# Kernel optimization log

Hardware: AMD Instinct MI355X
Metric: run time of the kernel (lower is better)

The kernel has to match this reference:

```python
import jax, jax.numpy as jnp
import numpy as np
import math

B, T, C = 2, 2048, 1024
H = 16
D = C // H  # 64


def setup_inputs() -> dict:
    key = jax.random.key(0)
    ks = jax.random.split(key, 5)
    s = 0.02
    return {
        "x": jax.random.normal(ks[0], (B, T, C), dtype=jnp.float32),
        "Wqkv": jax.random.normal(ks[1], (C, 3 * C), dtype=jnp.float32) * s,
        "bqkv": jax.random.normal(ks[2], (3 * C,), dtype=jnp.float32) * s,
        "Wo": jax.random.normal(ks[3], (C, C), dtype=jnp.float32) * s,
        "bo": jax.random.normal(ks[4], (C,), dtype=jnp.float32) * s,
    }


def reference(x, Wqkv, bqkv, Wo, bo):
    b, t, c = x.shape
    qkv = x @ Wqkv + bqkv                      # [B,T,3C]
    qkv = qkv.reshape(b, t, 3, H, D)           # split (three h d) as in einops pattern
    q = jnp.transpose(qkv[:, :, 0], (0, 2, 1, 3))  # [B,H,T,D]
    k = jnp.transpose(qkv[:, :, 1], (0, 2, 1, 3))
    v = jnp.transpose(qkv[:, :, 2], (0, 2, 1, 3))
    e = jnp.einsum('bhqd,bhkd->bhqk', q, k) * (1.0 / math.sqrt(D))  # [B,H,T,T]
    causal = jnp.tril(jnp.ones((t, t), dtype=bool))
    e = jnp.where(causal[None, None, :, :], e, -jnp.inf)
    a = jax.nn.softmax(e, axis=-1)             # attention dropout = identity (eval)
    y = jnp.einsum('bhqk,bhkd->bhqd', a, v)    # [B,H,T,D]
    y = jnp.transpose(y, (0, 2, 1, 3)).reshape(b, t, c)
    return y @ Wo + bo                         # resid dropout = identity (eval)
```

## Files before the change

### kernel.cpp

```cpp
#include <hip/hip_runtime.h>
#include <math.h>

#define Bn 2
#define Tn 2048
#define Cn 1024
#define Hn 16
#define Dn 64

typedef short  bf16x8 __attribute__((ext_vector_type(8)));
typedef short  s16x4  __attribute__((ext_vector_type(4)));
typedef float  f32x4  __attribute__((ext_vector_type(4)));

static __device__ __forceinline__ unsigned short f32_bf16(float f) {
    unsigned u = __float_as_uint(f);
    return (unsigned short)((u + 0x7fffu + ((u >> 16) & 1u)) >> 16);
}
static __device__ __forceinline__ float bf16_f32(unsigned short h) {
    return __uint_as_float(((unsigned)h) << 16);
}
static __device__ __forceinline__ void split_store(short* dh, short* dl, float4 v) {
    unsigned short h0 = f32_bf16(v.x), h1 = f32_bf16(v.y),
                   h2 = f32_bf16(v.z), h3 = f32_bf16(v.w);
    *(s16x4*)dh = (s16x4){(short)h0, (short)h1, (short)h2, (short)h3};
    *(s16x4*)dl = (s16x4){(short)f32_bf16(v.x - bf16_f32(h0)),
                          (short)f32_bf16(v.y - bf16_f32(h1)),
                          (short)f32_bf16(v.z - bf16_f32(h2)),
                          (short)f32_bf16(v.w - bf16_f32(h3))};
}

__global__ __launch_bounds__(256) void gemm_mfma3(const float* __restrict__ A,
                                                  const float* __restrict__ B,
                                                  const float* __restrict__ bias,
                                                  float* __restrict__ C,
                                                  int M, int N, int K) {
    __shared__ short Ah[128][40];
    __shared__ short Al[128][40];
    __shared__ short Bh[128][40];
    __shared__ short Bl[128][40];

    const int tid = threadIdx.x;
    const int m0 = blockIdx.y * 128;
    const int n0 = blockIdx.x * 128;
    const int w  = tid >> 6;
    const int l  = tid & 63;
    const int wr = w >> 1;
    const int wc = w & 1;
    const int lr = l & 15;
    const int g8 = (l >> 4) * 8;

    const int a_in  = tid & 7;
    const int a_r0  = tid >> 3;
    const int q     = tid >> 2;
    const int e     = tid & 3;
    const int b_n   = 4 * (q & 31);
    const int b_kb  = 16 * (q >> 5);

    f32x4 acc[4][4];
    #pragma unroll
    for (int i = 0; i < 4; ++i)
        #pragma unroll
        for (int j = 0; j < 4; ++j)
            acc[i][j] = (f32x4){0.f, 0.f, 0.f, 0.f};

    for (int k0 = 0; k0 < K; k0 += 32) {
        #pragma unroll
        for (int c4 = 0; c4 < 4; ++c4) {
            const int row = a_r0 + 32 * c4;
            const float4 v = *(const float4*)(A + (size_t)(m0 + row) * K + k0 + 4 * a_in);
            split_store(&Ah[row][4 * a_in], &Al[row][4 * a_in], v);
        }
        #pragma unroll
        for (int c = 0; c < 4; ++c) {
            const int krow = b_kb + 4 * c + e;
            const float4 v = *(const float4*)(B + (size_t)(k0 + krow) * N + n0 + b_n);
            float4 b1, u, b2, t;
            b1.x = __shfl_xor(v.x, 1); b1.y = __shfl_xor(v.y, 1);
            b1.z = __shfl_xor(v.z, 1); b1.w = __shfl_xor(v.w, 1);
            if (e & 1) { u.x = b1.y; u.y = v.y; u.z = b1.w; u.w = v.w; }
            else       { u.x = v.x;  u.y = b1.x; u.z = v.z; u.w = b1.z; }
            b2.x = __shfl_xor(u.x, 2); b2.y = __shfl_xor(u.y, 2);
            b2.z = __shfl_xor(u.z, 2); b2.w = __shfl_xor(u.w, 2);
            if (e & 2) { t.x = b2.z; t.y = b2.w; t.z = u.z; t.w = u.w; }
            else       { t.x = u.x;  t.y = u.y;  t.z = b2.x; t.w = b2.y; }
            const int nrow = b_n + e;
            const int kcol = b_kb + 4 * c;
            split_store(&Bh[nrow][kcol], &Bl[nrow][kcol], t);
        }
        __syncthreads();

        bf16x8 fah[4], fal[4], fbh[4], fbl[4];
        #pragma unroll
        for (int i = 0; i < 4; ++i) {
            fah[i] = *(const bf16x8*)&Ah[64 * wr + 16 * i + lr][g8];
            fal[i] = *(const bf16x8*)&Al[64 * wr + 16 * i + lr][g8];
            fbh[i] = *(const bf16x8*)&Bh[64 * wc + 16 * i + lr][g8];
            fbl[i] = *(const bf16x8*)&Bl[64 * wc + 16 * i + lr][g8];
        }
        #pragma unroll
        for (int i = 0; i < 4; ++i)
            #pragma unroll
            for (int j = 0; j < 4; ++j) {
                acc[i][j] = __builtin_amdgcn_mfma_f32_16x16x32_bf16(fah[i], fbh[j], acc[i][j], 0, 0, 0);
                acc[i][j] = __builtin_amdgcn_mfma_f32_16x16x32_bf16(fah[i], fbl[j], acc[i][j], 0, 0, 0);
                acc[i][j] = __builtin_amdgcn_mfma_f32_16x16x32_bf16(fal[i], fbh[j], acc[i][j], 0, 0, 0);
            }
        __syncthreads();
    }

    #pragma unroll
    for (int j = 0; j < 4; ++j) {
        const int col = n0 + 64 * wc + 16 * j + lr;
        const float bv = bias[col];
        #pragma unroll
        for (int i = 0; i < 4; ++i) {
            const int rbase = m0 + 64 * wr + 16 * i + (l >> 4) * 4;
            #pragma unroll
            for (int r = 0; r < 4; ++r)
                C[(size_t)(rbase + r) * N + col] = acc[i][j][r] + bv;
        }
    }
}

__global__ __launch_bounds__(256) void attn_mfma(const float* __restrict__ qkv,
                                                 float* __restrict__ y) {
    __shared__ short K_h[64][72], K_l[64][72];
    __shared__ short V_h[64][72], V_l[64][72];
    __shared__ short P_h[4][16][72], P_l[4][16][72];

    const int tid = threadIdx.x;
    const int w   = tid >> 6;
    const int ln  = tid & 63;
    const int g   = ln >> 4;
    const int c16 = ln & 15;

    const int bid = blockIdx.x;
    const int p   = bid & 31;
    const int qt  = 31 - (bid >> 5);
    const int b   = p >> 4;
    const int h   = p & 15;

    const float* base = qkv + (size_t)b * (Tn * 3 * Cn) + h * Dn;

    {
        const int r  = tid >> 2;
        const int c4 = 4 * (tid & 3);
        #pragma unroll
        for (int c = 0; c < 4; ++c) {
            const int col = c4 + 16 * c;
            const float4 v = *(const float4*)(base + (size_t)(64 * qt + r) * (3 * Cn) + col);
            split_store(&K_h[r][col], &K_l[r][col], v);
        }
    }
    __syncthreads();
    bf16x8 qh[2], ql[2];
    qh[0] = *(const bf16x8*)&K_h[16 * w + c16][8 * g];
    qh[1] = *(const bf16x8*)&K_h[16 * w + c16][32 + 8 * g];
    ql[0] = *(const bf16x8*)&K_l[16 * w + c16][8 * g];
    ql[1] = *(const bf16x8*)&K_l[16 * w + c16][32 + 8 * g];
    __syncthreads();

    f32x4 Y[4];
    #pragma unroll
    for (int j = 0; j < 4; ++j) Y[j] = (f32x4){0.f, 0.f, 0.f, 0.f};
    float m[4]    = {-INFINITY, -INFINITY, -INFINITY, -INFINITY};
    float lsum[4] = {0.f, 0.f, 0.f, 0.f};

    for (int kt = 0; kt <= qt; ++kt) {
        {
            const int r  = tid >> 2;
            const int c4 = 4 * (tid & 3);
            #pragma unroll
            for (int c = 0; c < 4; ++c) {
                const int col = c4 + 16 * c;
                const float4 v = *(const float4*)(base + Cn + (size_t)(64 * kt + r) * (3 * Cn) + col);
                split_store(&K_h[r][col], &K_l[r][col], v);
            }
        }
        {
            const int q2 = tid >> 2, e = tid & 3;
            const int kb = 4 * (q2 & 15);
            const int db = 16 * (q2 >> 4);
            #pragma unroll
            for (int c = 0; c < 4; ++c) {
                const int d4 = db + 4 * c;
                const float4 v = *(const float4*)(base + 2 * Cn + (size_t)(64 * kt + kb + e) * (3 * Cn) + d4);
                float4 b1, u, b2, t;
                b1.x = __shfl_xor(v.x, 1); b1.y = __shfl_xor(v.y, 1);
                b1.z = __shfl_xor(v.z, 1); b1.w = __shfl_xor(v.w, 1);
                if (e & 1) { u.x = b1.y; u.y = v.y; u.z = b1.w; u.w = v.w; }
                else       { u.x = v.x;  u.y = b1.x; u.z = v.z; u.w = b1.z; }
                b2.x = __shfl_xor(u.x, 2); b2.y = __shfl_xor(u.y, 2);
                b2.z = __shfl_xor(u.z, 2); b2.w = __shfl_xor(u.w, 2);
                if (e & 2) { t.x = b2.z; t.y = b2.w; t.z = u.z; t.w = u.w; }
                else       { t.x = u.x;  t.y = u.y;  t.z = b2.x; t.w = b2.y; }
                split_store(&V_h[d4 + e][kb], &V_l[d4 + e][kb], t);
            }
        }
        __syncthreads();

        f32x4 sa[4];
        #pragma unroll
        for (int t = 0; t < 4; ++t) sa[t] = (f32x4){0.f, 0.f, 0.f, 0.f};
        #pragma unroll
        for (int t = 0; t < 4; ++t) {
            const bf16x8 kh0 = *(const bf16x8*)&K_h[16 * t + c16][8 * g];
            const bf16x8 kh1 = *(const bf16x8*)&K_h[16 * t + c16][32 + 8 * g];
            const bf16x8 kl0 = *(const bf16x8*)&K_l[16 * t + c16][8 * g];
            const bf16x8 kl1 = *(const bf16x8*)&K_l[16 * t + c16][32 + 8 * g];
            sa[t] = __builtin_amdgcn_mfma_f32_16x16x32_bf16(qh[0], kh0, sa[t], 0, 0, 0);
            sa[t] = __builtin_amdgcn_mfma_f32_16x16x32_bf16(qh[1], kh1, sa[t], 0, 0, 0);
            sa[t] = __builtin_amdgcn_mfma_f32_16x16x32_bf16(qh[0], kl0, sa[t], 0, 0, 0);
            sa[t] = __builtin_amdgcn_mfma_f32_16x16x32_bf16(qh[1], kl1, sa[t], 0, 0, 0);
            sa[t] = __builtin_amdgcn_mfma_f32_16x16x32_bf16(ql[0], kh0, sa[t], 0, 0, 0);
            sa[t] = __builtin_amdgcn_mfma_f32_16x16x32_bf16(ql[1], kh1, sa[t], 0, 0, 0);
        }

        const bool diag = (kt == qt);
        float sc[4][4];
        #pragma unroll
        for (int t = 0; t < 4; ++t)
            #pragma unroll
            for (int r = 0; r < 4; ++r) {
                float v = sa[t][r] * 0.125f;
                if (diag && (16 * t + c16 > 16 * w + 4 * g + r)) v = -INFINITY;
                sc[t][r] = v;
            }
        #pragma unroll
        for (int r = 0; r < 4; ++r) {
            float mt = fmaxf(fmaxf(sc[0][r], sc[1][r]), fmaxf(sc[2][r], sc[3][r]));
            mt = fmaxf(mt, __shfl_xor(mt, 1));
            mt = fmaxf(mt, __shfl_xor(mt, 2));
            mt = fmaxf(mt, __shfl_xor(mt, 4));
            mt = fmaxf(mt, __shfl_xor(mt, 8));
            const float mnew = fmaxf(m[r], mt);
            const float corr = __expf(m[r] - mnew);
            m[r] = mnew;
            float rs = 0.f;
            #pragma unroll
            for (int t = 0; t < 4; ++t) {
                const float pe = __expf(sc[t][r] - mnew);
                sc[t][r] = pe;
                rs += pe;
            }
            rs += __shfl_xor(rs, 1);
            rs += __shfl_xor(rs, 2);
            rs += __shfl_xor(rs, 4);
            rs += __shfl_xor(rs, 8);
            lsum[r] = lsum[r] * corr + rs;
            #pragma unroll
            for (int j = 0; j < 4; ++j) Y[j][r] *= corr;
        }

        #pragma unroll
        for (int t = 0; t < 4; ++t)
            #pragma unroll
            for (int r = 0; r < 4; ++r) {
                const unsigned short ph = f32_bf16(sc[t][r]);
                const unsigned short pl = f32_bf16(sc[t][r] - bf16_f32(ph));
                P_h[w][4 * g + r][16 * t + c16] = (short)ph;
                P_l[w][4 * g + r][16 * t + c16] = (short)pl;
            }

        bf16x8 pfh[2], pfl[2];
        pfh[0] = *(const bf16x8*)&P_h[w][c16][8 * g];
        pfh[1] = *(const bf16x8*)&P_h[w][c16][32 + 8 * g];
        pfl[0] = *(const bf16x8*)&P_l[w][c16][8 * g];
        pfl[1] = *(const bf16x8*)&P_l[w][c16][32 + 8 * g];
        #pragma unroll
        for (int j = 0; j < 4; ++j) {
            #pragma unroll
            for (int kc = 0; kc < 2; ++kc) {
                const bf16x8 vh = *(const bf16x8*)&V_h[16 * j + c16][32 * kc + 8 * g];
                const bf16x8 vl = *(const bf16x8*)&V_l[16 * j + c16][32 * kc + 8 * g];
                Y[j] = __builtin_amdgcn_mfma_f32_16x16x32_bf16(pfh[kc], vh, Y[j], 0, 0, 0);
                Y[j] = __builtin_amdgcn_mfma_f32_16x16x32_bf16(pfh[kc], vl, Y[j], 0, 0, 0);
                Y[j] = __builtin_amdgcn_mfma_f32_16x16x32_bf16(pfl[kc], vh, Y[j], 0, 0, 0);
            }
        }
        __syncthreads();
    }

    float* yb = y + (size_t)(b * Tn + 64 * qt) * Cn + h * Dn;
    #pragma unroll
    for (int r = 0; r < 4; ++r) {
        const float inv = 1.f / lsum[r];
        #pragma unroll
        for (int j = 0; j < 4; ++j)
            yb[(size_t)(16 * w + 4 * g + r) * Cn + 16 * j + c16] = Y[j][r] * inv;
    }
}

extern "C" void kernel_launch(void* const* d_in, const int* in_sizes, int n_in,
                              void* d_out, int out_size, void* d_ws, size_t ws_size,
                              hipStream_t stream) {
    const float* x    = (const float*)d_in[0];
    const float* Wqkv = (const float*)d_in[1];
    const float* bqkv = (const float*)d_in[2];
    const float* Wo   = (const float*)d_in[3];
    const float* bo   = (const float*)d_in[4];
    float* out = (float*)d_out;

    const int M = Bn * Tn;
    float* qkv = (float*)d_ws;
    float* yat = qkv + (size_t)M * (3 * Cn);

    {
        dim3 grid((3 * Cn) / 128, M / 128), blk(256);
        gemm_mfma3<<<grid, blk, 0, stream>>>(x, Wqkv, bqkv, qkv, M, 3 * Cn, Cn);
    }
    {
        dim3 grid(1024), blk(256);
        attn_mfma<<<grid, blk, 0, stream>>>(qkv, yat);
    }
    {
        dim3 grid(Cn / 128, M / 128), blk(256);
        gemm_mfma3<<<grid, blk, 0, stream>>>(yat, Wo, bo, out, M, Cn, Cn);
    }
}
```

Measured before the change: 424.0 us.

## Emit pre-split bf16 K and transposed V from QKV GEMM; attention reads fragments directly

The QKV GEMM epilogue now writes Q as fp32 and K and V as pre-split bf16 hi/lo pairs, with K in head-major layout and V transposed. The attention kernel then loads MFMA fragments straight from global memory and no longer stages K/V in shared memory or syncs per tile. Each block now handles 128 queries (32 per wave) instead of 64, so every K/V fragment load feeds twice as many MFMAs. In exchange the epilogue scatters uncoalesced scalar stores, attention issues redundant global/L2 loads across waves, and there is less block-level parallelism.

```diff
diff --git a/kernel.cpp b/kernel.cpp
--- a/kernel.cpp
+++ b/kernel.cpp
@@ -28,11 +28,15 @@
                           (short)f32_bf16(v.w - bf16_f32(h3))};
 }
 
-__global__ __launch_bounds__(256) void gemm_mfma3(const float* __restrict__ A,
-                                                  const float* __restrict__ B,
-                                                  const float* __restrict__ bias,
-                                                  float* __restrict__ C,
-                                                  int M, int N, int K) {
+__global__ __launch_bounds__(256) void gemm_qkv(const float* __restrict__ A,
+                                                const float* __restrict__ B,
+                                                const float* __restrict__ bias,
+                                                float* __restrict__ qbuf,
+                                                short* __restrict__ kh_,
+                                                short* __restrict__ kl_,
+                                                short* __restrict__ vth_,
+                                                short* __restrict__ vtl_) {
+    const int M = 4096, N = 3072, K = 1024;
     __shared__ short Ah[128][40];
     __shared__ short Al[128][40];
     __shared__ short Bh[128][40];
@@ -107,6 +111,142 @@
         __syncthreads();
     }
 
+    const int region = n0 >> 10;
+    if (region == 0) {
+        #pragma unroll
+        for (int j = 0; j < 4; ++j) {
+            const int col = n0 + 64 * wc + 16 * j + lr;
+            const float bv = bias[col];
+            #pragma unroll
+            for (int i = 0; i < 4; ++i) {
+                const int rbase = m0 + 64 * wr + 16 * i + (l >> 4) * 4;
+                #pragma unroll
+                for (int r = 0; r < 4; ++r)
+                    qbuf[(size_t)(rbase + r) * 1024 + col] = acc[i][j][r] + bv;
+            }
+        }
+    } else if (region == 1) {
+        #pragma unroll
+        for (int j = 0; j < 4; ++j) {
+            const int colg = n0 + 64 * wc + 16 * j + lr;
+            const int colp = colg - 1024;
+            const int h = colp >> 6, d = colp & 63;
+            const float bv = bias[colg];
+            #pragma unroll
+            for (int i = 0; i < 4; ++i) {
+                const int rbase = m0 + 64 * wr + 16 * i + (l >> 4) * 4;
+                const int b  = rbase >> 11;
+                const int t0 = rbase & 2047;
+                const size_t base = ((size_t)(b * Hn + h) * Tn + t0) * 64 + d;
+                #pragma unroll
+                for (int r = 0; r < 4; ++r) {
+                    const float v = acc[i][j][r] + bv;
+                    const unsigned short hh = f32_bf16(v);
+                    kh_[base + (size_t)r * 64] = (short)hh;
+                    kl_[base + (size_t)r * 64] = (short)f32_bf16(v - bf16_f32(hh));
+                }
+            }
+        }
+    } else {
+        #pragma unroll
+        for (int j = 0; j < 4; ++j) {
+            const int colg = n0 + 64 * wc + 16 * j + lr;
+            const int colp = colg - 2048;
+            const int h = colp >> 6, d = colp & 63;
+            const float bv = bias[colg];
+            #pragma unroll
+            for (int i = 0; i < 4; ++i) {
+                const int rbase = m0 + 64 * wr + 16 * i + (l >> 4) * 4;
+                const int b  = rbase >> 11;
+                const int t0 = rbase & 2047;
+                float4 v4 = {acc[i][j][0] + bv, acc[i][j][1] + bv,
+                             acc[i][j][2] + bv, acc[i][j][3] + bv};
+                const size_t base = ((size_t)(b * Hn + h) * 64 + d) * Tn + t0;
+                split_store(vth_ + base, vtl_ + base, v4);
+            }
+        }
+    }
+}
+
+__global__ __launch_bounds__(256) void gemm_mfma3(const float* __restrict__ A,
+                                                  const float* __restrict__ B,
+                                                  const float* __restrict__ bias,
+                                                  float* __restrict__ C,
+                                                  int M, int N, int K) {
+    __shared__ short Ah[128][40];
+    __shared__ short Al[128][40];
+    __shared__ short Bh[128][40];
+    __shared__ short Bl[128][40];
+
+    const int tid = threadIdx.x;
+    const int m0 = blockIdx.y * 128;
+    const int n0 = blockIdx.x * 128;
+    const int w  = tid >> 6;
+    const int l  = tid & 63;
+    const int wr = w >> 1;
+    const int wc = w & 1;
+    const int lr = l & 15;
+    const int g8 = (l >> 4) * 8;
+
+    const int a_in  = tid & 7;
+    const int a_r0  = tid >> 3;
+    const int q     = tid >> 2;
+    const int e     = tid & 3;
+    const int b_n   = 4 * (q & 31);
+    const int b_kb  = 16 * (q >> 5);
+
+    f32x4 acc[4][4];
+    #pragma unroll
+    for (int i = 0; i < 4; ++i)
+        #pragma unroll
+        for (int j = 0; j < 4; ++j)
+            acc[i][j] = (f32x4){0.f, 0.f, 0.f, 0.f};
+
+    for (int k0 = 0; k0 < K; k0 += 32) {
+        #pragma unroll
+        for (int c4 = 0; c4 < 4; ++c4) {
+            const int row = a_r0 + 32 * c4;
+            const float4 v = *(const float4*)(A + (size_t)(m0 + row) * K + k0 + 4 * a_in);
+            split_store(&Ah[row][4 * a_in], &Al[row][4 * a_in], v);
+        }
+        #pragma unroll
+        for (int c = 0; c < 4; ++c) {
+            const int krow = b_kb + 4 * c + e;
+            const float4 v = *(const float4*)(B + (size_t)(k0 + krow) * N + n0 + b_n);
+            float4 b1, u, b2, t;
+            b1.x = __shfl_xor(v.x, 1); b1.y = __shfl_xor(v.y, 1);
+            b1.z = __shfl_xor(v.z, 1); b1.w = __shfl_xor(v.w, 1);
+            if (e & 1) { u.x = b1.y; u.y = v.y; u.z = b1.w; u.w = v.w; }
+            else       { u.x = v.x;  u.y = b1.x; u.z = v.z; u.w = b1.z; }
+            b2.x = __shfl_xor(u.x, 2); b2.y = __shfl_xor(u.y, 2);
+            b2.z = __shfl_xor(u.z, 2); b2.w = __shfl_xor(u.w, 2);
+            if (e & 2) { t.x = b2.z; t.y = b2.w; t.z = u.z; t.w = u.w; }
+            else       { t.x = u.x;  t.y = u.y;  t.z = b2.x; t.w = b2.y; }
+            const int nrow = b_n + e;
+            const int kcol = b_kb + 4 * c;
+            split_store(&Bh[nrow][kcol], &Bl[nrow][kcol], t);
+        }
+        __syncthreads();
+
+        bf16x8 fah[4], fal[4], fbh[4], fbl[4];
+        #pragma unroll
+        for (int i = 0; i < 4; ++i) {
+            fah[i] = *(const bf16x8*)&Ah[64 * wr + 16 * i + lr][g8];
+            fal[i] = *(const bf16x8*)&Al[64 * wr + 16 * i + lr][g8];
+            fbh[i] = *(const bf16x8*)&Bh[64 * wc + 16 * i + lr][g8];
+            fbl[i] = *(const bf16x8*)&Bl[64 * wc + 16 * i + lr][g8];
+        }
+        #pragma unroll
+        for (int i = 0; i < 4; ++i)
+            #pragma unroll
+            for (int j = 0; j < 4; ++j) {
+                acc[i][j] = __builtin_amdgcn_mfma_f32_16x16x32_bf16(fah[i], fbh[j], acc[i][j], 0, 0, 0);
+                acc[i][j] = __builtin_amdgcn_mfma_f32_16x16x32_bf16(fah[i], fbl[j], acc[i][j], 0, 0, 0);
+                acc[i][j] = __builtin_amdgcn_mfma_f32_16x16x32_bf16(fal[i], fbh[j], acc[i][j], 0, 0, 0);
+            }
+        __syncthreads();
+    }
+
     #pragma unroll
     for (int j = 0; j < 4; ++j) {
         const int col = n0 + 64 * wc + 16 * j + lr;
@@ -121,11 +261,13 @@
     }
 }
 
-__global__ __launch_bounds__(256) void attn_mfma(const float* __restrict__ qkv,
-                                                 float* __restrict__ y) {
-    __shared__ short K_h[64][72], K_l[64][72];
-    __shared__ short V_h[64][72], V_l[64][72];
-    __shared__ short P_h[4][16][72], P_l[4][16][72];
+__global__ __launch_bounds__(256) void attn_mfma2(const float* __restrict__ qbuf,
+                                                  const short* __restrict__ kh_,
+                                                  const short* __restrict__ kl_,
+                                                  const short* __restrict__ vth_,
+                                                  const short* __restrict__ vtl_,
+                                                  float* __restrict__ y) {
+    __shared__ short Ph[128][72], Pl[128][72];
 
     const int tid = threadIdx.x;
     const int w   = tid >> 6;
@@ -135,159 +277,165 @@
 
     const int bid = blockIdx.x;
     const int p   = bid & 31;
-    const int qt  = 31 - (bid >> 5);
+    const int qb  = 15 - (bid >> 5);
     const int b   = p >> 4;
     const int h   = p & 15;
 
-    const float* base = qkv + (size_t)b * (Tn * 3 * Cn) + h * Dn;
-
     {
-        const int r  = tid >> 2;
-        const int c4 = 4 * (tid & 3);
-        #pragma unroll
-        for (int c = 0; c < 4; ++c) {
-            const int col = c4 + 16 * c;
-            const float4 v = *(const float4*)(base + (size_t)(64 * qt + r) * (3 * Cn) + col);
-            split_store(&K_h[r][col], &K_l[r][col], v);
+        const int row = tid >> 1;
+        const int ch  = (tid & 1) * 32;
+        const float* qp = qbuf + (size_t)(b * Tn + 128 * qb + row) * Cn + h * Dn + ch;
+        #pragma unroll
+        for (int cc = 0; cc < 8; ++cc) {
+            const float4 v = *(const float4*)(qp + 4 * cc);
+            split_store(&Ph[row][ch + 4 * cc], &Pl[row][ch + 4 * cc], v);
         }
     }
     __syncthreads();
-    bf16x8 qh[2], ql[2];
-    qh[0] = *(const bf16x8*)&K_h[16 * w + c16][8 * g];
-    qh[1] = *(const bf16x8*)&K_h[16 * w + c16][32 + 8 * g];
-    ql[0] = *(const bf16x8*)&K_l[16 * w + c16][8 * g];
-    ql[1] = *(const bf16x8*)&K_l[16 * w + c16][32 + 8 * g];
+    bf16x8 qh[2][2], ql[2][2];
+    #pragma unroll
+    for (int a = 0; a < 2; ++a) {
+        const int row = 32 * w + 16 * a + c16;
+        qh[a][0] = *(const bf16x8*)&Ph[row][8 * g];
+        qh[a][1] = *(const bf16x8*)&Ph[row][32 + 8 * g];
+        ql[a][0] = *(const bf16x8*)&Pl[row][8 * g];
+        ql[a][1] = *(const bf16x8*)&Pl[row][32 + 8 * g];
+    }
     __syncthreads();
 
-    f32x4 Y[4];
-    #pragma unroll
-    for (int j = 0; j < 4; ++j) Y[j] = (f32x4){0.f, 0.f, 0.f, 0.f};
-    float m[4]    = {-INFINITY, -INFINITY, -INFINITY, -INFINITY};
-    float lsum[4] = {0.f, 0.f, 0.f, 0.f};
-
-    for (int kt = 0; kt <= qt; ++kt) {
-        {
-            const int r  = tid >> 2;
-            const int c4 = 4 * (tid & 3);
-            #pragma unroll
-            for (int c = 0; c < 4; ++c) {
-                const int col = c4 + 16 * c;
-                const float4 v = *(const float4*)(base + Cn + (size_t)(64 * kt + r) * (3 * Cn) + col);
-                split_store(&K_h[r][col], &K_l[r][col], v);
-            }
-        }
-        {
-            const int q2 = tid >> 2, e = tid & 3;
-            const int kb = 4 * (q2 & 15);
-            const int db = 16 * (q2 >> 4);
-            #pragma unroll
-            for (int c = 0; c < 4; ++c) {
-                const int d4 = db + 4 * c;
-                const float4 v = *(const float4*)(base + 2 * Cn + (size_t)(64 * kt + kb + e) * (3 * Cn) + d4);
-                float4 b1, u, b2, t;
-                b1.x = __shfl_xor(v.x, 1); b1.y = __shfl_xor(v.y, 1);
-                b1.z = __shfl_xor(v.z, 1); b1.w = __shfl_xor(v.w, 1);
-                if (e & 1) { u.x = b1.y; u.y = v.y; u.z = b1.w; u.w = v.w; }
-                else       { u.x = v.x;  u.y = b1.x; u.z = v.z; u.w = b1.z; }
-                b2.x = __shfl_xor(u.x, 2); b2.y = __shfl_xor(u.y, 2);
-                b2.z = __shfl_xor(u.z, 2); b2.w = __shfl_xor(u.w, 2);
-                if (e & 2) { t.x = b2.z; t.y = b2.w; t.z = u.z; t.w = u.w; }
-                else       { t.x = u.x;  t.y = u.y;  t.z = b2.x; t.w = b2.y; }
-                split_store(&V_h[d4 + e][kb], &V_l[d4 + e][kb], t);
-            }
-        }
-        __syncthreads();
-
-        f32x4 sa[4];
-        #pragma unroll
-        for (int t = 0; t < 4; ++t) sa[t] = (f32x4){0.f, 0.f, 0.f, 0.f};
+    f32x4 Y[2][4];
+    float m[2][4], lsum[2][4];
+    #pragma unroll
+    for (int a = 0; a < 2; ++a)
+        #pragma unroll
+        for (int j = 0; j < 4; ++j) Y[a][j] = (f32x4){0.f, 0.f, 0.f, 0.f};
+    #pragma unroll
+    for (int a = 0; a < 2; ++a)
+        #pragma unroll
+        for (int r = 0; r < 4; ++r) { m[a][r] = -INFINITY; lsum[a][r] = 0.f; }
+
+    const size_t kvbase = (size_t)(b * Hn + h);
+    const short* kbh = kh_  + kvbase * Tn * 64;
+    const short* kbl = kl_  + kvbase * Tn * 64;
+    const short* vbh = vth_ + kvbase * 64 * Tn;
+    const short* vbl = vtl_ + kvbase * 64 * Tn;
+
+    const int qwave  = 128 * qb + 32 * w;
+    const int ntiles = (qwave + 31) / 64 + 1;
+
+    for (int kt = 0; kt < ntiles; ++kt) {
+        f32x4 sa[2][4];
+        #pragma unroll
+        for (int a = 0; a < 2; ++a)
+            #pragma unroll
+            for (int t = 0; t < 4; ++t) sa[a][t] = (f32x4){0.f, 0.f, 0.f, 0.f};
         #pragma unroll
         for (int t = 0; t < 4; ++t) {
-            const bf16x8 kh0 = *(const bf16x8*)&K_h[16 * t + c16][8 * g];
-            const bf16x8 kh1 = *(const bf16x8*)&K_h[16 * t + c16][32 + 8 * g];
-            const bf16x8 kl0 = *(const bf16x8*)&K_l[16 * t + c16][8 * g];
-            const bf16x8 kl1 = *(const bf16x8*)&K_l[16 * t + c16][32 + 8 * g];
-            sa[t] = __builtin_amdgcn_mfma_f32_16x16x32_bf16(qh[0], kh0, sa[t], 0, 0, 0);
-            sa[t] = __builtin_amdgcn_mfma_f32_16x16x32_bf16(qh[1], kh1, sa[t], 0, 0, 0);
-            sa[t] = __builtin_amdgcn_mfma_f32_16x16x32_bf16(qh[0], kl0, sa[t], 0, 0, 0);
-            sa[t] = __builtin_amdgcn_mfma_f32_16x16x32_bf16(qh[1], kl1, sa[t], 0, 0, 0);
-            sa[t] = __builtin_amdgcn_mfma_f32_16x16x32_bf16(ql[0], kh0, sa[t], 0, 0, 0);
-            sa[t] = __builtin_amdgcn_mfma_f32_16x16x32_bf16(ql[1], kh1, sa[t], 0, 0, 0);
-        }
-
-        const bool diag = (kt == qt);
-        float sc[4][4];
-        #pragma unroll
-        for (int t = 0; t < 4; ++t)
+            const size_t krow = (size_t)(64 * kt + 16 * t + c16) * 64;
+            const bf16x8 kh0 = *(const bf16x8*)(kbh + krow + 8 * g);
+            const bf16x8 kh1 = *(const bf16x8*)(kbh + krow + 32 + 8 * g);
+            const bf16x8 kl0 = *(const bf16x8*)(kbl + krow + 8 * g);
+            const bf16x8 kl1 = *(const bf16x8*)(kbl + krow + 32 + 8 * g);
+            #pragma unroll
+            for (int a = 0; a < 2; ++a) {
+                sa[a][t] = __builtin_amdgcn_mfma_f32_16x16x32_bf16(qh[a][0], kh0, sa[a][t], 0, 0, 0);
+                sa[a][t] = __builtin_amdgcn_mfma_f32_16x16x32_bf16(qh[a][1], kh1, sa[a][t], 0, 0, 0);
+                sa[a][t] = __builtin_amdgcn_mfma_f32_16x16x32_bf16(qh[a][0], kl0, sa[a][t], 0, 0, 0);
+                sa[a][t] = __builtin_amdgcn_mfma_f32_16x16x32_bf16(qh[a][1], kl1, sa[a][t], 0, 0, 0);
+                sa[a][t] = __builtin_amdgcn_mfma_f32_16x16x32_bf16(ql[a][0], kh0, sa[a][t], 0, 0, 0);
+                sa[a][t] = __builtin_amdgcn_mfma_f32_16x16x32_bf16(ql[a][1], kh1, sa[a][t], 0, 0, 0);
+            }
+        }
+
+        #pragma unroll
+        for (int a = 0; a < 2; ++a)
+            #pragma unroll
+            for (int t = 0; t < 4; ++t)
+                #pragma unroll
+                for (int r = 0; r < 4; ++r) {
+                    float v = sa[a][t][r] * 0.125f;
+                    if (64 * kt + 16 * t + c16 > qwave + 16 * a + 4 * g + r)
+                        v = -INFINITY;
+                    sa[a][t][r] = v;
+                }
+        #pragma unroll
+        for (int a = 0; a < 2; ++a)
             #pragma unroll
             for (int r = 0; r < 4; ++r) {
-                float v = sa[t][r] * 0.125f;
-                if (diag && (16 * t + c16 > 16 * w + 4 * g + r)) v = -INFINITY;
-                sc[t][r] = v;
-            }
+                float mt = fmaxf(fmaxf(sa[a][0][r], sa[a][1][r]),
+                                 fmaxf(sa[a][2][r], sa[a][3][r]));
+                mt = fmaxf(mt, __shfl_xor(mt, 1));
+                mt = fmaxf(mt, __shfl_xor(mt, 2));
+                mt = fmaxf(mt, __shfl_xor(mt, 4));
+                mt = fmaxf(mt, __shfl_xor(mt, 8));
+                const float mnew = fmaxf(m[a][r], mt);
+                const float corr = __expf(m[a][r] - mnew);
+                m[a][r] = mnew;
+                float rs = 0.f;
+                #pragma unroll
+                for (int t = 0; t < 4; ++t) {
+                    const float pe = __expf(sa[a][t][r] - mnew);
+                    sa[a][t][r] = pe;
+                    rs += pe;
+                }
+                rs += __shfl_xor(rs, 1);
+                rs += __shfl_xor(rs, 2);
+                rs += __shfl_xor(rs, 4);
+                rs += __shfl_xor(rs, 8);
+                lsum[a][r] = lsum[a][r] * corr + rs;
+                #pragma unroll
+                for (int j = 0; j < 4; ++j) Y[a][j][r] *= corr;
+            }
+
+        #pragma unroll
+        for (int a = 0; a < 2; ++a)
+            #pragma unroll
+            for (int t = 0; t < 4; ++t)
+                #pragma unroll
+                for (int r = 0; r < 4; ++r) {
+                    const float pv = sa[a][t][r];
+                    const unsigned short ph = f32_bf16(pv);
+                    Ph[32 * w + 16 * a + 4 * g + r][16 * t + c16] = (short)ph;
+                    Pl[32 * w + 16 * a + 4 * g + r][16 * t + c16] =
+                        (short)f32_bf16(pv - bf16_f32(ph));
+                }
+        bf16x8 pfh[2][2], pfl[2][2];
+        #pragma unroll
+        for (int a = 0; a < 2; ++a) {
+            const int row = 32 * w + 16 * a + c16;
+            pfh[a][0] = *(const bf16x8*)&Ph[row][8 * g];
+            pfh[a][1] = *(const bf16x8*)&Ph[row][32 + 8 * g];
+            pfl[a][0] = *(const bf16x8*)&Pl[row][8 * g];
+            pfl[a][1] = *(const bf16x8*)&Pl[row][32 + 8 * g];
+        }
+
+        #pragma unroll
+        for (int j = 0; j < 4; ++j) {
+            const size_t vrow = (size_t)(16 * j + c16) * Tn + 64 * kt;
+            #pragma unroll
+            for (int kc = 0; kc < 2; ++kc) {
+                const bf16x8 vh = *(const bf16x8*)(vbh + vrow + 32 * kc + 8 * g);
+                const bf16x8 vl = *(const bf16x8*)(vbl + vrow + 32 * kc + 8 * g);
+                #pragma unroll
+                for (int a = 0; a < 2; ++a) {
+                    Y[a][j] = __builtin_amdgcn_mfma_f32_16x16x32_bf16(pfh[a][kc], vh, Y[a][j], 0, 0, 0);
+                    Y[a][j] = __builtin_amdgcn_mfma_f32_16x16x32_bf16(pfh[a][kc], vl, Y[a][j], 0, 0, 0);
+                    Y[a][j] = __builtin_amdgcn_mfma_f32_16x16x32_bf16(pfl[a][kc], vh, Y[a][j], 0, 0, 0);
+                }
+            }
+        }
+    }
+
+    #pragma unroll
+    for (int a = 0; a < 2; ++a)
         #pragma unroll
         for (int r = 0; r < 4; ++r) {
-            float mt = fmaxf(fmaxf(sc[0][r], sc[1][r]), fmaxf(sc[2][r], sc[3][r]));
-            mt = fmaxf(mt, __shfl_xor(mt, 1));
-            mt = fmaxf(mt, __shfl_xor(mt, 2));
-            mt = fmaxf(mt, __shfl_xor(mt, 4));
-            mt = fmaxf(mt, __shfl_xor(mt, 8));
-            const float mnew = fmaxf(m[r], mt);
-            const float corr = __expf(m[r] - mnew);
-            m[r] = mnew;
-            float rs = 0.f;
-            #pragma unroll
-            for (int t = 0; t < 4; ++t) {
-                const float pe = __expf(sc[t][r] - mnew);
-                sc[t][r] = pe;
-                rs += pe;
-            }
-            rs += __shfl_xor(rs, 1);
-            rs += __shfl_xor(rs, 2);
-            rs += __shfl_xor(rs, 4);
-            rs += __shfl_xor(rs, 8);
-            lsum[r] = lsum[r] * corr + rs;
-            #pragma unroll
-            for (int j = 0; j < 4; ++j) Y[j][r] *= corr;
-        }
-
-        #pragma unroll
-        for (int t = 0; t < 4; ++t)
-            #pragma unroll
-            for (int r = 0; r < 4; ++r) {
-                const unsigned short ph = f32_bf16(sc[t][r]);
-                const unsigned short pl = f32_bf16(sc[t][r] - bf16_f32(ph));
-                P_h[w][4 * g + r][16 * t + c16] = (short)ph;
-                P_l[w][4 * g + r][16 * t + c16] = (short)pl;
-            }
-
-        bf16x8 pfh[2], pfl[2];
-        pfh[0] = *(const bf16x8*)&P_h[w][c16][8 * g];
-        pfh[1] = *(const bf16x8*)&P_h[w][c16][32 + 8 * g];
-        pfl[0] = *(const bf16x8*)&P_l[w][c16][8 * g];
-        pfl[1] = *(const bf16x8*)&P_l[w][c16][32 + 8 * g];
-        #pragma unroll
-        for (int j = 0; j < 4; ++j) {
-            #pragma unroll
-            for (int kc = 0; kc < 2; ++kc) {
-                const bf16x8 vh = *(const bf16x8*)&V_h[16 * j + c16][32 * kc + 8 * g];
-                const bf16x8 vl = *(const bf16x8*)&V_l[16 * j + c16][32 * kc + 8 * g];
-                Y[j] = __builtin_amdgcn_mfma_f32_16x16x32_bf16(pfh[kc], vh, Y[j], 0, 0, 0);
-                Y[j] = __builtin_amdgcn_mfma_f32_16x16x32_bf16(pfh[kc], vl, Y[j], 0, 0, 0);
-                Y[j] = __builtin_amdgcn_mfma_f32_16x16x32_bf16(pfl[kc], vh, Y[j], 0, 0, 0);
-            }
-        }
-        __syncthreads();
-    }
-
-    float* yb = y + (size_t)(b * Tn + 64 * qt) * Cn + h * Dn;
-    #pragma unroll
-    for (int r = 0; r < 4; ++r) {
-        const float inv = 1.f / lsum[r];
-        #pragma unroll
-        for (int j = 0; j < 4; ++j)
-            yb[(size_t)(16 * w + 4 * g + r) * Cn + 16 * j + c16] = Y[j][r] * inv;
-    }
+            const float inv = 1.f / lsum[a][r];
+            const int row = qwave + 16 * a + 4 * g + r;
+            #pragma unroll
+            for (int j = 0; j < 4; ++j)
+                y[(size_t)(b * Tn + row) * Cn + h * Dn + 16 * j + c16] = Y[a][j][r] * inv;
+        }
 }
 
 extern "C" void kernel_launch(void* const* d_in, const int* in_sizes, int n_in,
@@ -301,16 +449,20 @@
     float* out = (float*)d_out;
 
     const int M = Bn * Tn;
-    float* qkv = (float*)d_ws;
-    float* yat = qkv + (size_t)M * (3 * Cn);
+    float* qbuf = (float*)d_ws;
+    float* yat  = qbuf + (size_t)M * Cn;
+    short* kh   = (short*)(yat + (size_t)M * Cn);
+    short* kl   = kh  + (size_t)Bn * Hn * Tn * 64;
+    short* vth  = kl  + (size_t)Bn * Hn * Tn * 64;
+    short* vtl  = vth + (size_t)Bn * Hn * Tn * 64;
 
     {
-        dim3 grid((3 * Cn) / 128, M / 128), blk(256);
-        gemm_mfma3<<<grid, blk, 0, stream>>>(x, Wqkv, bqkv, qkv, M, 3 * Cn, Cn);
+        dim3 grid(3072 / 128, M / 128), blk(256);
+        gemm_qkv<<<grid, blk, 0, stream>>>(x, Wqkv, bqkv, qbuf, kh, kl, vth, vtl);
     }
     {
-        dim3 grid(1024), blk(256);
-        attn_mfma<<<grid, blk, 0, stream>>>(qkv, yat);
+        dim3 grid(512), blk(256);
+        attn_mfma2<<<grid, blk, 0, stream>>>(qbuf, kh, kl, vth, vtl, yat);
     }
     {
         dim3 grid(Cn / 128, M / 128), blk(256);
```

New measurement: 566.3 us. +33.6%, slower.
